# Kernel tuning notes

Hardware: AMD Instinct MI355X
Metric: run time of the kernel (lower is better)

## Reference

```python
import jax, jax.numpy as jnp
import numpy as np

# Forest of B complete binary trees, depth DEPTH (root at level 0, leaves at level DEPTH)
B = 16
DEPTH = 14
NPT = 2 ** (DEPTH + 1) - 1   # nodes per tree = 32767
N = B * NPT                  # total nodes = 524272
X = 128                      # x_size
H = 128                      # h_size
NC = 10                      # num_classes


def _tree_levels():
    """Static tree structure: per internal level, (node_ids, children_ids[.,2]); plus leaf ids."""
    offs = np.arange(B, dtype=np.int64)[:, None] * NPT
    levels = []
    for l in range(DEPTH):  # internal levels 0..DEPTH-1
        n = np.arange(2 ** l - 1, 2 ** (l + 1) - 1, dtype=np.int64)
        ch = np.stack([2 * n + 1, 2 * n + 2], axis=1)
        nodes = (n[None, :] + offs).reshape(-1)
        children = (ch[None, :, :] + offs[:, :, None]).reshape(-1, 2)
        levels.append((nodes, children))
    leaf = np.arange(2 ** DEPTH - 1, NPT, dtype=np.int64)
    leaves = (leaf[None, :] + offs).reshape(-1)
    return levels, leaves


def _apply_node(iou, c_in):
    # iou: [M, 3H]; chunk order i, o, u as in torch.chunk(iou, 3, 1)
    i, o, u = jnp.split(iou, 3, axis=-1)
    c = jax.nn.sigmoid(i) * jnp.tanh(u) + c_in
    h = jax.nn.sigmoid(o) * jnp.tanh(c)
    return h, c


def setup_inputs() -> dict:
    key = jax.random.key(0)
    ks = jax.random.split(key, 8)
    rn = lambda k, shp, sc: jax.random.normal(k, shp, dtype=jnp.float32) * sc
    return {
        "feature": rn(ks[0], (N, X), 1.0),
        "h": rn(ks[1], (N, H), 1.0),
        "c": rn(ks[2], (N, H), 1.0),
        "W_iou": rn(ks[3], (3 * H, X), 0.05),
        "U_iou": rn(ks[4], (3 * H, H), 0.05),
        "b_iou": jnp.zeros((1, 3 * H), jnp.float32),
        "U_f_w": rn(ks[5], (H, H), 0.05),
        "U_f_b": jnp.zeros((H,), jnp.float32),
        "W_lin": rn(ks[6], (NC, H), 0.05),
        "b_lin": jnp.zeros((NC,), jnp.float32),
    }


def reference(feature, h, c, W_iou, U_iou, b_iou, U_f_w, U_f_b, W_lin, b_lin):
    levels, leaves = _tree_levels()

    # Leaves: no mailbox -> iou = W_iou(x) + b_iou, c stays initial c
    iou_leaf = feature[leaves] @ W_iou.T + b_iou
    h_leaf, c_leaf = _apply_node(iou_leaf, c[leaves])
    h = h.at[leaves].set(h_leaf)
    c = c.at[leaves].set(c_leaf)

    # Internal levels bottom-up (topological order)
    for nodes, children in reversed(levels):
        hc = h[children]                                  # [M, 2, H]
        cc = c[children]                                  # [M, 2, H]
        h_tild = hc.sum(axis=1)                           # child-sum
        f = jax.nn.sigmoid(jnp.einsum('mkh,gh->mkg', hc, U_f_w) + U_f_b)
        c_agg = (f * cc).sum(axis=1)
        # DGL reduce OVERWRITES 'iou': internal nodes use U_iou(h_tild) only
        iou = h_tild @ U_iou.T + b_iou
        h_new, c_new = _apply_node(iou, c_agg)
        h = h.at[nodes].set(h_new)
        c = c.at[nodes].set(c_new)

    # AvgPooling over each graph's nodes, then classifier
    hg = h.reshape(B, NPT, H).mean(axis=1)
    logits = hg @ W_lin.T + b_lin
    return jax.nn.log_softmax(logits, axis=-1)
```

## Files before the change

### kernel.cpp

```cpp
#include <hip/hip_runtime.h>
#include <hip/hip_bf16.h>
#include <stdint.h>

#define NTREES 16
#define TDEPTH 14
#define NPT    32767
#define HDIM   128

typedef __bf16 bf16x8 __attribute__((ext_vector_type(8)));
typedef float  f32x4  __attribute__((ext_vector_type(4)));

__device__ __forceinline__ float fsig(float x) {
    return __builtin_amdgcn_rcpf(1.0f + __expf(-x));
}
__device__ __forceinline__ float ftanh(float x) {
    return 1.0f - 2.0f * __builtin_amdgcn_rcpf(__expf(2.0f * x) + 1.0f);
}

__global__ __launch_bounds__(256) void prep_kernel(
    const float* __restrict__ W_iou, const float* __restrict__ U_iou,
    const float* __restrict__ U_f,
    __bf16* __restrict__ wiou_bf, __bf16* __restrict__ uiou_bf,
    __bf16* __restrict__ uf_bf, float* __restrict__ hg)
{
    int idx = blockIdx.x * 256 + threadIdx.x;
    if (idx < 49152)       wiou_bf[idx]          = (__bf16)W_iou[idx];
    else if (idx < 98304)  uiou_bf[idx - 49152]  = (__bf16)U_iou[idx - 49152];
    else if (idx < 114688) uf_bf[idx - 98304]    = (__bf16)U_f[idx - 98304];
    else if (idx < 116736) hg[idx - 114688]      = 0.0f;
}

__global__ __launch_bounds__(256) void leaf_kernel(
    const float* __restrict__ feat, float* __restrict__ c,
    const __bf16* __restrict__ wiou_bf, const float* __restrict__ b_iou,
    __bf16* __restrict__ hbf)
{
    __shared__ __align__(16) __bf16 As[128 * 128];
    const int t = threadIdx.x;
    const int blk = blockIdx.x;
    const int tree = blk >> 7, chunk = blk & 127;
    const int rowbase = tree * NPT + 16383 + chunk * 128;

    for (int idx = t; idx < 128 * 32; idx += 256) {
        int r = idx >> 5, c4 = idx & 31;
        const float4 v = *reinterpret_cast<const float4*>(
            feat + (size_t)(rowbase + r) * HDIM + c4 * 4);
        int u16 = (c4 >> 1) ^ (r & 7);
        __bf16* dst = As + r * 128 + u16 * 8 + (c4 & 1) * 4;
        dst[0] = (__bf16)v.x; dst[1] = (__bf16)v.y;
        dst[2] = (__bf16)v.z; dst[3] = (__bf16)v.w;
    }
    __syncthreads();

    const int wave = t >> 6, lane = t & 63;
    const int n15 = lane & 15, q = lane >> 4;
    int aoff[4];
    #pragma unroll
    for (int kk = 0; kk < 4; ++kk) aoff[kk] = ((kk * 4 + q) ^ (n15 & 7)) * 8;

    for (int jj = 0; jj < 2; ++jj) {
        const int jg = wave + jj * 4;
        bf16x8 bfr[3][4];
        #pragma unroll
        for (int p = 0; p < 3; ++p) {
            const __bf16* bp = wiou_bf + (size_t)(p * 128 + jg * 16 + n15) * HDIM + q * 8;
            #pragma unroll
            for (int kk = 0; kk < 4; ++kk)
                bfr[p][kk] = *reinterpret_cast<const bf16x8*>(bp + kk * 32);
        }
        const int j = jg * 16 + n15;
        const float bi = b_iou[j], bo = b_iou[128 + j], bu = b_iou[256 + j];
        for (int mt = 0; mt < 8; ++mt) {
            bf16x8 afr[4];
            #pragma unroll
            for (int kk = 0; kk < 4; ++kk)
                afr[kk] = *reinterpret_cast<const bf16x8*>(As + (mt * 16 + n15) * 128 + aoff[kk]);
            f32x4 ai = {0,0,0,0}, ao = {0,0,0,0}, au = {0,0,0,0};
            #pragma unroll
            for (int kk = 0; kk < 4; ++kk) {
                ai = __builtin_amdgcn_mfma_f32_16x16x32_bf16(afr[kk], bfr[0][kk], ai, 0,0,0);
                ao = __builtin_amdgcn_mfma_f32_16x16x32_bf16(afr[kk], bfr[1][kk], ao, 0,0,0);
                au = __builtin_amdgcn_mfma_f32_16x16x32_bf16(afr[kk], bfr[2][kk], au, 0,0,0);
            }
            #pragma unroll
            for (int reg = 0; reg < 4; ++reg) {
                int r = mt * 16 + q * 4 + reg;
                size_t off = (size_t)(rowbase + r) * HDIM + j;
                float ci = c[off];
                float cn = fsig(ai[reg] + bi) * ftanh(au[reg] + bu) + ci;
                float hn = fsig(ao[reg] + bo) * ftanh(cn);
                c[off]   = cn;
                hbf[off] = (__bf16)hn;
            }
        }
    }
}

__global__ __launch_bounds__(256) void level_kernel(
    int l, int Mlev,
    float* __restrict__ c,
    const __bf16* __restrict__ uiou_bf, const __bf16* __restrict__ uf_bf,
    const float* __restrict__ b_iou, const float* __restrict__ ufb,
    __bf16* __restrict__ hbf)
{
    __shared__ __align__(16) __bf16 Hc[64 * 128];
    __shared__ __align__(16) __bf16 Ht[32 * 128];
    __shared__ float cagg[32 * 132];
    const int t = threadIdx.x;
    const int blk32 = blockIdx.x * 32;
    const int nmask = (1 << l) - 1;

    for (int idx = t; idx < 64 * 16; idx += 256) {
        int r = idx >> 4, s = idx & 15;
        int inode = blk32 + (r >> 1);
        uint4 v = {0, 0, 0, 0};
        if (inode < Mlev) {
            int tree = inode >> l, local = inode & nmask;
            int nloc = nmask + local;
            size_t crow = (size_t)tree * NPT + 2 * nloc + 1 + (r & 1);
            v = *reinterpret_cast<const uint4*>(hbf + crow * HDIM + s * 8);
        }
        *reinterpret_cast<uint4*>(Hc + r * 128 + ((s ^ (r & 7)) * 8)) = v;
    }
    __syncthreads();

    for (int idx = t; idx < 32 * 16; idx += 256) {
        int nno = idx >> 4, s = idx & 15;
        const __bf16* p0 = Hc + (2 * nno)     * 128 + ((s ^ ((2 * nno) & 7)) * 8);
        const __bf16* p1 = Hc + (2 * nno + 1) * 128 + ((s ^ ((2 * nno + 1) & 7)) * 8);
        __bf16* po = Ht + nno * 128 + ((s ^ (nno & 7)) * 8);
        #pragma unroll
        for (int e = 0; e < 8; ++e) po[e] = (__bf16)((float)p0[e] + (float)p1[e]);
    }
    __syncthreads();

    const int wave = t >> 6, lane = t & 63;
    const int n15 = lane & 15, q = lane >> 4;
    int aoff[4];
    #pragma unroll
    for (int kk = 0; kk < 4; ++kk) aoff[kk] = ((kk * 4 + q) ^ (n15 & 7)) * 8;

    {
        bf16x8 bfr[2][4];
        #pragma unroll
        for (int i = 0; i < 2; ++i) {
            int nt = wave + i * 4;
            const __bf16* bp = uf_bf + (size_t)(nt * 16 + n15) * HDIM + q * 8;
            #pragma unroll
            for (int kk = 0; kk < 4; ++kk)
                bfr[i][kk] = *reinterpret_cast<const bf16x8*>(bp + kk * 32);
        }
        for (int mt = 0; mt < 4; ++mt) {
            bf16x8 afr[4];
            #pragma unroll
            for (int kk = 0; kk < 4; ++kk)
                afr[kk] = *reinterpret_cast<const bf16x8*>(Hc + (mt * 16 + n15) * 128 + aoff[kk]);
            f32x4 acc0 = {0,0,0,0}, acc1 = {0,0,0,0};
            #pragma unroll
            for (int kk = 0; kk < 4; ++kk) {
                acc0 = __builtin_amdgcn_mfma_f32_16x16x32_bf16(afr[kk], bfr[0][kk], acc0, 0,0,0);
                acc1 = __builtin_amdgcn_mfma_f32_16x16x32_bf16(afr[kk], bfr[1][kk], acc1, 0,0,0);
            }
            #pragma unroll
            for (int i = 0; i < 2; ++i) {
                int nt = wave + i * 4;
                int j = nt * 16 + n15;
                float fb = ufb[j];
                f32x4 acc = i ? acc1 : acc0;
                #pragma unroll
                for (int p = 0; p < 2; ++p) {
                    int nl = mt * 8 + q * 2 + p;
                    int inode = blk32 + nl;
                    if (inode < Mlev) {
                        int tree = inode >> l, local = inode & nmask;
                        int nloc = nmask + local;
                        size_t crow = (size_t)tree * NPT + 2 * nloc + 1;
                        float c0 = c[crow * HDIM + j];
                        float c1 = c[(crow + 1) * HDIM + j];
                        float f0 = fsig(acc[2 * p] + fb);
                        float f1 = fsig(acc[2 * p + 1] + fb);
                        cagg[nl * 132 + j] = f0 * c0 + f1 * c1;
                    }
                }
            }
        }
    }
    __syncthreads();

    for (int jj = 0; jj < 2; ++jj) {
        const int jg = wave + jj * 4;
        bf16x8 bfr[3][4];
        #pragma unroll
        for (int p = 0; p < 3; ++p) {
            const __bf16* bp = uiou_bf + (size_t)(p * 128 + jg * 16 + n15) * HDIM + q * 8;
            #pragma unroll
            for (int kk = 0; kk < 4; ++kk)
                bfr[p][kk] = *reinterpret_cast<const bf16x8*>(bp + kk * 32);
        }
        const int j = jg * 16 + n15;
        const float bi = b_iou[j], bo = b_iou[128 + j], bu = b_iou[256 + j];
        for (int mt = 0; mt < 2; ++mt) {
            bf16x8 afr[4];
            #pragma unroll
            for (int kk = 0; kk < 4; ++kk)
                afr[kk] = *reinterpret_cast<const bf16x8*>(Ht + (mt * 16 + n15) * 128 + aoff[kk]);
            f32x4 ai = {0,0,0,0}, ao = {0,0,0,0}, au = {0,0,0,0};
            #pragma unroll
            for (int kk = 0; kk < 4; ++kk) {
                ai = __builtin_amdgcn_mfma_f32_16x16x32_bf16(afr[kk], bfr[0][kk], ai, 0,0,0);
                ao = __builtin_amdgcn_mfma_f32_16x16x32_bf16(afr[kk], bfr[1][kk], ao, 0,0,0);
                au = __builtin_amdgcn_mfma_f32_16x16x32_bf16(afr[kk], bfr[2][kk], au, 0,0,0);
            }
            #pragma unroll
            for (int reg = 0; reg < 4; ++reg) {
                int nl = mt * 16 + q * 4 + reg;
                int inode = blk32 + nl;
                if (inode < Mlev) {
                    int tree = inode >> l, local = inode & nmask;
                    int nloc = nmask + local;
                    size_t nrow = (size_t)tree * NPT + nloc;
                    float cg = cagg[nl * 132 + j];
                    float cn = fsig(ai[reg] + bi) * ftanh(au[reg] + bu) + cg;
                    float hn = fsig(ao[reg] + bo) * ftanh(cn);
                    c[nrow * HDIM + j]   = cn;
                    hbf[nrow * HDIM + j] = (__bf16)hn;
                }
            }
        }
    }
}

__global__ __launch_bounds__(256) void pool_kernel(
    const __bf16* __restrict__ hbf, float* __restrict__ hg)
{
    const int t = threadIdx.x;
    const int tree = blockIdx.x >> 6, chunk = blockIdx.x & 63;
    const int col = t & 127, rg = t >> 7;
    const int r0 = chunk * 512;
    const int r1 = (r0 + 512 < NPT) ? (r0 + 512) : NPT;
    float s = 0.0f;
    for (int row = r0 + rg; row < r1; row += 2)
        s += (float)hbf[((size_t)tree * NPT + row) * HDIM + col];
    atomicAdd(&hg[tree * HDIM + col], s);
}

__global__ __launch_bounds__(256) void cls_kernel(
    const float* __restrict__ hg, const float* __restrict__ W_lin,
    const float* __restrict__ b_lin, float* __restrict__ out)
{
    __shared__ float lg[16 * 10];
    const int t = threadIdx.x;
    if (t < 160) {
        int b = t / 10, cc = t % 10;
        float s = b_lin[cc];
        const float inv = 1.0f / 32767.0f;
        for (int j = 0; j < HDIM; ++j)
            s += hg[b * HDIM + j] * inv * W_lin[cc * HDIM + j];
        lg[b * 10 + cc] = s;
    }
    __syncthreads();
    if (t < 16) {
        float m = lg[t * 10];
        for (int i = 1; i < 10; ++i) m = fmaxf(m, lg[t * 10 + i]);
        float sum = 0.0f;
        for (int i = 0; i < 10; ++i) sum += __expf(lg[t * 10 + i] - m);
        float lse = __logf(sum) + m;
        for (int i = 0; i < 10; ++i) out[t * 10 + i] = lg[t * 10 + i] - lse;
    }
}

extern "C" void kernel_launch(void* const* d_in, const int* in_sizes, int n_in,
                              void* d_out, int out_size, void* d_ws, size_t ws_size,
                              hipStream_t stream)
{
    const float* feat  = (const float*)d_in[0];
    char*        hbase = (char*)d_in[1];
    float*       c     = (float*)d_in[2];
    const float* W_iou = (const float*)d_in[3];
    const float* U_iou = (const float*)d_in[4];
    const float* b_iou = (const float*)d_in[5];
    const float* U_f_w = (const float*)d_in[6];
    const float* U_f_b = (const float*)d_in[7];
    const float* W_lin = (const float*)d_in[8];
    const float* b_lin = (const float*)d_in[9];

    __bf16* hbf = (__bf16*)hbase;
    const size_t WOFF = 134217728;
    __bf16* wiou_bf = (__bf16*)(hbase + WOFF);
    __bf16* uiou_bf = (__bf16*)(hbase + WOFF + 98304);
    __bf16* uf_bf   = (__bf16*)(hbase + WOFF + 196608);
    float*  hg      = (float*)(hbase + WOFF + 229376);

    prep_kernel<<<456, 256, 0, stream>>>(W_iou, U_iou, U_f_w, wiou_bf, uiou_bf, uf_bf, hg);
    leaf_kernel<<<2048, 256, 0, stream>>>(feat, c, wiou_bf, b_iou, hbf);
    for (int l = TDEPTH - 1; l >= 0; --l) {
        int Mlev = NTREES << l;
        int grid = (Mlev + 31) / 32;
        level_kernel<<<grid, 256, 0, stream>>>(l, Mlev, c, uiou_bf, uf_bf, b_iou, U_f_b, hbf);
    }
    pool_kernel<<<1024, 256, 0, stream>>>(hbf, hg);
    cls_kernel<<<1, 256, 0, stream>>>(hg, W_lin, b_lin, (float*)d_out);
}
```

Baseline: 1.165 ms.

## Fuse leaves and two lowest internal levels in shared memory, fuse pooling and tail levels

```diff
diff --git a/kernel.cpp b/kernel.cpp
--- a/kernel.cpp
+++ b/kernel.cpp
@@ -3,9 +3,7 @@
 #include <stdint.h>
 
 #define NTREES 16
-#define TDEPTH 14
 #define NPT    32767
-#define HDIM   128
 
 typedef __bf16 bf16x8 __attribute__((ext_vector_type(8)));
 typedef float  f32x4  __attribute__((ext_vector_type(4)));
@@ -15,6 +13,9 @@
 }
 __device__ __forceinline__ float ftanh(float x) {
     return 1.0f - 2.0f * __builtin_amdgcn_rcpf(__expf(2.0f * x) + 1.0f);
+}
+__device__ __forceinline__ int swz(int r, int j) {
+    return r * 128 + (((j >> 3) ^ (r & 7)) << 3) + (j & 7);
 }
 
 __global__ __launch_bounds__(256) void prep_kernel(
@@ -30,47 +31,62 @@
     else if (idx < 116736) hg[idx - 114688]      = 0.0f;
 }
 
-__global__ __launch_bounds__(256) void leaf_kernel(
-    const float* __restrict__ feat, float* __restrict__ c,
-    const __bf16* __restrict__ wiou_bf, const float* __restrict__ b_iou,
-    __bf16* __restrict__ hbf)
+__global__ __launch_bounds__(256) void mega_kernel(
+    const float* __restrict__ feat, const float* __restrict__ c0g,
+    const __bf16* __restrict__ wiou, const __bf16* __restrict__ uiou,
+    const __bf16* __restrict__ uf,
+    const float* __restrict__ b_iou, const float* __restrict__ ufb,
+    __bf16* __restrict__ hbf, __bf16* __restrict__ cbf, float* __restrict__ hg)
 {
-    __shared__ __align__(16) __bf16 As[128 * 128];
+    __shared__ __align__(16) __bf16 HA[64 * 128];
+    __shared__ __align__(16) __bf16 CA[64 * 136];
+    __shared__ __align__(16) unsigned char Sbuf[8192 + 32 * 132 * 4];
+    __bf16* As   = (__bf16*)Sbuf;
+    __bf16* Ht   = (__bf16*)Sbuf;
+    float*  cagg = (float*)(Sbuf + 8192);
+
     const int t = threadIdx.x;
-    const int blk = blockIdx.x;
-    const int tree = blk >> 7, chunk = blk & 127;
-    const int rowbase = tree * NPT + 16383 + chunk * 128;
-
-    for (int idx = t; idx < 128 * 32; idx += 256) {
+    const int tree = blockIdx.x >> 8, sub = blockIdx.x & 255;
+    const size_t leafrow = (size_t)tree * NPT + 16383 + (size_t)sub * 64;
+
+    for (int idx = t; idx < 64 * 32; idx += 256) {
         int r = idx >> 5, c4 = idx & 31;
-        const float4 v = *reinterpret_cast<const float4*>(
-            feat + (size_t)(rowbase + r) * HDIM + c4 * 4);
-        int u16 = (c4 >> 1) ^ (r & 7);
-        __bf16* dst = As + r * 128 + u16 * 8 + (c4 & 1) * 4;
-        dst[0] = (__bf16)v.x; dst[1] = (__bf16)v.y;
-        dst[2] = (__bf16)v.z; dst[3] = (__bf16)v.w;
-    }
-    __syncthreads();
-
-    const int wave = t >> 6, lane = t & 63;
-    const int n15 = lane & 15, q = lane >> 4;
+        float4 v = *reinterpret_cast<const float4*>(feat + (leafrow + r) * 128 + c4 * 4);
+        __bf16* dst = As + r * 128 + (((c4 >> 1) ^ (r & 7)) << 3) + ((c4 & 1) << 2);
+        dst[0] = (__bf16)v.x; dst[1] = (__bf16)v.y; dst[2] = (__bf16)v.z; dst[3] = (__bf16)v.w;
+    }
+    __syncthreads();
+
+    const int wave = t >> 6, lane = t & 63, n15 = lane & 15, q = lane >> 4;
     int aoff[4];
     #pragma unroll
-    for (int kk = 0; kk < 4; ++kk) aoff[kk] = ((kk * 4 + q) ^ (n15 & 7)) * 8;
-
+    for (int kk = 0; kk < 4; ++kk) aoff[kk] = ((kk * 4 + q) ^ (n15 & 7)) << 3;
+    float hsum0 = 0.f, hsum1 = 0.f;
+
+    bf16x8 ufr[2][4];
+    float fb[2];
+    #pragma unroll
+    for (int i = 0; i < 2; ++i) {
+        int nt = wave + i * 4;
+        const __bf16* bp = uf + (size_t)(nt * 16 + n15) * 128 + q * 8;
+        #pragma unroll
+        for (int kk = 0; kk < 4; ++kk) ufr[i][kk] = *reinterpret_cast<const bf16x8*>(bp + kk * 32);
+        fb[i] = ufb[nt * 16 + n15];
+    }
+
+    #pragma unroll
     for (int jj = 0; jj < 2; ++jj) {
         const int jg = wave + jj * 4;
         bf16x8 bfr[3][4];
         #pragma unroll
         for (int p = 0; p < 3; ++p) {
-            const __bf16* bp = wiou_bf + (size_t)(p * 128 + jg * 16 + n15) * HDIM + q * 8;
-            #pragma unroll
-            for (int kk = 0; kk < 4; ++kk)
-                bfr[p][kk] = *reinterpret_cast<const bf16x8*>(bp + kk * 32);
+            const __bf16* bp = wiou + (size_t)(p * 128 + jg * 16 + n15) * 128 + q * 8;
+            #pragma unroll
+            for (int kk = 0; kk < 4; ++kk) bfr[p][kk] = *reinterpret_cast<const bf16x8*>(bp + kk * 32);
         }
         const int j = jg * 16 + n15;
         const float bi = b_iou[j], bo = b_iou[128 + j], bu = b_iou[256 + j];
-        for (int mt = 0; mt < 8; ++mt) {
+        for (int mt = 0; mt < 4; ++mt) {
             bf16x8 afr[4];
             #pragma unroll
             for (int kk = 0; kk < 4; ++kk)
@@ -85,23 +101,169 @@
             #pragma unroll
             for (int reg = 0; reg < 4; ++reg) {
                 int r = mt * 16 + q * 4 + reg;
-                size_t off = (size_t)(rowbase + r) * HDIM + j;
-                float ci = c[off];
+                float ci = c0g[(leafrow + r) * 128 + j];
                 float cn = fsig(ai[reg] + bi) * ftanh(au[reg] + bu) + ci;
                 float hn = fsig(ao[reg] + bo) * ftanh(cn);
-                c[off]   = cn;
-                hbf[off] = (__bf16)hn;
-            }
-        }
-    }
+                HA[swz(r, j)]    = (__bf16)hn;
+                CA[r * 136 + j]  = (__bf16)cn;
+                if (jj == 0) hsum0 += hn; else hsum1 += hn;
+            }
+        }
+    }
+    __syncthreads();
+
+    for (int idx = t; idx < 32 * 16; idx += 256) {
+        int nno = idx >> 4, s = idx & 15;
+        const __bf16* p0 = HA + (2 * nno) * 128     + (((s ^ ((2 * nno) & 7))) << 3);
+        const __bf16* p1 = HA + (2 * nno + 1) * 128 + (((s ^ ((2 * nno + 1) & 7))) << 3);
+        __bf16* po = Ht + nno * 128 + (((s ^ (nno & 7))) << 3);
+        #pragma unroll
+        for (int e = 0; e < 8; ++e) po[e] = (__bf16)((float)p0[e] + (float)p1[e]);
+    }
+    for (int mt = 0; mt < 4; ++mt) {
+        bf16x8 afr[4];
+        #pragma unroll
+        for (int kk = 0; kk < 4; ++kk)
+            afr[kk] = *reinterpret_cast<const bf16x8*>(HA + (mt * 16 + n15) * 128 + aoff[kk]);
+        f32x4 a0 = {0,0,0,0}, a1 = {0,0,0,0};
+        #pragma unroll
+        for (int kk = 0; kk < 4; ++kk) {
+            a0 = __builtin_amdgcn_mfma_f32_16x16x32_bf16(afr[kk], ufr[0][kk], a0, 0,0,0);
+            a1 = __builtin_amdgcn_mfma_f32_16x16x32_bf16(afr[kk], ufr[1][kk], a1, 0,0,0);
+        }
+        #pragma unroll
+        for (int i = 0; i < 2; ++i) {
+            int j2 = (wave + i * 4) * 16 + n15;
+            f32x4 acc = i ? a1 : a0;
+            #pragma unroll
+            for (int p = 0; p < 2; ++p) {
+                int nl = mt * 8 + q * 2 + p;
+                float cc0 = (float)CA[(2 * nl) * 136 + j2];
+                float cc1 = (float)CA[(2 * nl + 1) * 136 + j2];
+                cagg[nl * 132 + j2] = fsig(acc[2*p] + fb[i]) * cc0 + fsig(acc[2*p+1] + fb[i]) * cc1;
+            }
+        }
+    }
+    __syncthreads();
+    #pragma unroll
+    for (int jj = 0; jj < 2; ++jj) {
+        const int jg = wave + jj * 4;
+        bf16x8 bfr[3][4];
+        #pragma unroll
+        for (int p = 0; p < 3; ++p) {
+            const __bf16* bp = uiou + (size_t)(p * 128 + jg * 16 + n15) * 128 + q * 8;
+            #pragma unroll
+            for (int kk = 0; kk < 4; ++kk) bfr[p][kk] = *reinterpret_cast<const bf16x8*>(bp + kk * 32);
+        }
+        const int j = jg * 16 + n15;
+        const float bi = b_iou[j], bo = b_iou[128 + j], bu = b_iou[256 + j];
+        for (int mt = 0; mt < 2; ++mt) {
+            bf16x8 afr[4];
+            #pragma unroll
+            for (int kk = 0; kk < 4; ++kk)
+                afr[kk] = *reinterpret_cast<const bf16x8*>(Ht + (mt * 16 + n15) * 128 + aoff[kk]);
+            f32x4 ai = {0,0,0,0}, ao = {0,0,0,0}, au = {0,0,0,0};
+            #pragma unroll
+            for (int kk = 0; kk < 4; ++kk) {
+                ai = __builtin_amdgcn_mfma_f32_16x16x32_bf16(afr[kk], bfr[0][kk], ai, 0,0,0);
+                ao = __builtin_amdgcn_mfma_f32_16x16x32_bf16(afr[kk], bfr[1][kk], ao, 0,0,0);
+                au = __builtin_amdgcn_mfma_f32_16x16x32_bf16(afr[kk], bfr[2][kk], au, 0,0,0);
+            }
+            #pragma unroll
+            for (int reg = 0; reg < 4; ++reg) {
+                int nl = mt * 16 + q * 4 + reg;
+                float cg = cagg[nl * 132 + j];
+                float cn = fsig(ai[reg] + bi) * ftanh(au[reg] + bu) + cg;
+                float hn = fsig(ao[reg] + bo) * ftanh(cn);
+                HA[swz(nl, j)]    = (__bf16)hn;
+                CA[nl * 136 + j]  = (__bf16)cn;
+                if (jj == 0) hsum0 += hn; else hsum1 += hn;
+            }
+        }
+    }
+    __syncthreads();
+
+    for (int idx = t; idx < 16 * 16; idx += 256) {
+        int nno = idx >> 4, s = idx & 15;
+        const __bf16* p0 = HA + (2 * nno) * 128     + (((s ^ ((2 * nno) & 7))) << 3);
+        const __bf16* p1 = HA + (2 * nno + 1) * 128 + (((s ^ ((2 * nno + 1) & 7))) << 3);
+        __bf16* po = Ht + nno * 128 + (((s ^ (nno & 7))) << 3);
+        #pragma unroll
+        for (int e = 0; e < 8; ++e) po[e] = (__bf16)((float)p0[e] + (float)p1[e]);
+    }
+    for (int mt = 0; mt < 2; ++mt) {
+        bf16x8 afr[4];
+        #pragma unroll
+        for (int kk = 0; kk < 4; ++kk)
+            afr[kk] = *reinterpret_cast<const bf16x8*>(HA + (mt * 16 + n15) * 128 + aoff[kk]);
+        f32x4 a0 = {0,0,0,0}, a1 = {0,0,0,0};
+        #pragma unroll
+        for (int kk = 0; kk < 4; ++kk) {
+            a0 = __builtin_amdgcn_mfma_f32_16x16x32_bf16(afr[kk], ufr[0][kk], a0, 0,0,0);
+            a1 = __builtin_amdgcn_mfma_f32_16x16x32_bf16(afr[kk], ufr[1][kk], a1, 0,0,0);
+        }
+        #pragma unroll
+        for (int i = 0; i < 2; ++i) {
+            int j2 = (wave + i * 4) * 16 + n15;
+            f32x4 acc = i ? a1 : a0;
+            #pragma unroll
+            for (int p = 0; p < 2; ++p) {
+                int nl = mt * 8 + q * 2 + p;
+                float cc0 = (float)CA[(2 * nl) * 136 + j2];
+                float cc1 = (float)CA[(2 * nl + 1) * 136 + j2];
+                cagg[nl * 132 + j2] = fsig(acc[2*p] + fb[i]) * cc0 + fsig(acc[2*p+1] + fb[i]) * cc1;
+            }
+        }
+    }
+    __syncthreads();
+    const size_t p12row = (size_t)tree * NPT + 4095 + (size_t)sub * 16;
+    #pragma unroll
+    for (int jj = 0; jj < 2; ++jj) {
+        const int jg = wave + jj * 4;
+        bf16x8 bfr[3][4];
+        #pragma unroll
+        for (int p = 0; p < 3; ++p) {
+            const __bf16* bp = uiou + (size_t)(p * 128 + jg * 16 + n15) * 128 + q * 8;
+            #pragma unroll
+            for (int kk = 0; kk < 4; ++kk) bfr[p][kk] = *reinterpret_cast<const bf16x8*>(bp + kk * 32);
+        }
+        const int j = jg * 16 + n15;
+        const float bi = b_iou[j], bo = b_iou[128 + j], bu = b_iou[256 + j];
+        bf16x8 afr[4];
+        #pragma unroll
+        for (int kk = 0; kk < 4; ++kk)
+            afr[kk] = *reinterpret_cast<const bf16x8*>(Ht + n15 * 128 + aoff[kk]);
+        f32x4 ai = {0,0,0,0}, ao = {0,0,0,0}, au = {0,0,0,0};
+        #pragma unroll
+        for (int kk = 0; kk < 4; ++kk) {
+            ai = __builtin_amdgcn_mfma_f32_16x16x32_bf16(afr[kk], bfr[0][kk], ai, 0,0,0);
+            ao = __builtin_amdgcn_mfma_f32_16x16x32_bf16(afr[kk], bfr[1][kk], ao, 0,0,0);
+            au = __builtin_amdgcn_mfma_f32_16x16x32_bf16(afr[kk], bfr[2][kk], au, 0,0,0);
+        }
+        #pragma unroll
+        for (int reg = 0; reg < 4; ++reg) {
+            int nl = q * 4 + reg;
+            float cg = cagg[nl * 132 + j];
+            float cn = fsig(ai[reg] + bi) * ftanh(au[reg] + bu) + cg;
+            float hn = fsig(ao[reg] + bo) * ftanh(cn);
+            cbf[(p12row + nl) * 128 + j] = (__bf16)cn;
+            hbf[(p12row + nl) * 128 + j] = (__bf16)hn;
+            if (jj == 0) hsum0 += hn; else hsum1 += hn;
+        }
+    }
+
+    float v = hsum0;
+    v += __shfl_xor(v, 16); v += __shfl_xor(v, 32);
+    if (lane < 16) atomicAdd(&hg[tree * 128 + wave * 16 + lane], v);
+    v = hsum1;
+    v += __shfl_xor(v, 16); v += __shfl_xor(v, 32);
+    if (lane < 16) atomicAdd(&hg[tree * 128 + (wave + 4) * 16 + lane], v);
 }
 
 __global__ __launch_bounds__(256) void level_kernel(
-    int l, int Mlev,
-    float* __restrict__ c,
-    const __bf16* __restrict__ uiou_bf, const __bf16* __restrict__ uf_bf,
+    int l, const __bf16* __restrict__ uiou, const __bf16* __restrict__ uf,
     const float* __restrict__ b_iou, const float* __restrict__ ufb,
-    __bf16* __restrict__ hbf)
+    __bf16* __restrict__ hbf, __bf16* __restrict__ cbf, float* __restrict__ hg)
 {
     __shared__ __align__(16) __bf16 Hc[64 * 128];
     __shared__ __align__(16) __bf16 Ht[32 * 128];
@@ -113,89 +275,74 @@
     for (int idx = t; idx < 64 * 16; idx += 256) {
         int r = idx >> 4, s = idx & 15;
         int inode = blk32 + (r >> 1);
-        uint4 v = {0, 0, 0, 0};
-        if (inode < Mlev) {
-            int tree = inode >> l, local = inode & nmask;
-            int nloc = nmask + local;
-            size_t crow = (size_t)tree * NPT + 2 * nloc + 1 + (r & 1);
-            v = *reinterpret_cast<const uint4*>(hbf + crow * HDIM + s * 8);
-        }
-        *reinterpret_cast<uint4*>(Hc + r * 128 + ((s ^ (r & 7)) * 8)) = v;
-    }
-    __syncthreads();
-
+        int tree = inode >> l, local = inode & nmask;
+        size_t crow = (size_t)tree * NPT + 2 * (nmask + local) + 1 + (r & 1);
+        uint4 v = *reinterpret_cast<const uint4*>(hbf + crow * 128 + s * 8);
+        *reinterpret_cast<uint4*>(Hc + r * 128 + ((s ^ (r & 7)) << 3)) = v;
+    }
+    __syncthreads();
     for (int idx = t; idx < 32 * 16; idx += 256) {
         int nno = idx >> 4, s = idx & 15;
-        const __bf16* p0 = Hc + (2 * nno)     * 128 + ((s ^ ((2 * nno) & 7)) * 8);
-        const __bf16* p1 = Hc + (2 * nno + 1) * 128 + ((s ^ ((2 * nno + 1) & 7)) * 8);
-        __bf16* po = Ht + nno * 128 + ((s ^ (nno & 7)) * 8);
+        const __bf16* p0 = Hc + (2 * nno) * 128     + (((s ^ ((2 * nno) & 7))) << 3);
+        const __bf16* p1 = Hc + (2 * nno + 1) * 128 + (((s ^ ((2 * nno + 1) & 7))) << 3);
+        __bf16* po = Ht + nno * 128 + (((s ^ (nno & 7))) << 3);
         #pragma unroll
         for (int e = 0; e < 8; ++e) po[e] = (__bf16)((float)p0[e] + (float)p1[e]);
     }
-    __syncthreads();
-
-    const int wave = t >> 6, lane = t & 63;
-    const int n15 = lane & 15, q = lane >> 4;
+
+    const int wave = t >> 6, lane = t & 63, n15 = lane & 15, q = lane >> 4;
     int aoff[4];
     #pragma unroll
-    for (int kk = 0; kk < 4; ++kk) aoff[kk] = ((kk * 4 + q) ^ (n15 & 7)) * 8;
-
-    {
-        bf16x8 bfr[2][4];
+    for (int kk = 0; kk < 4; ++kk) aoff[kk] = ((kk * 4 + q) ^ (n15 & 7)) << 3;
+    float hsum0 = 0.f, hsum1 = 0.f;
+
+    bf16x8 ufr[2][4];
+    float fb[2];
+    #pragma unroll
+    for (int i = 0; i < 2; ++i) {
+        int nt = wave + i * 4;
+        const __bf16* bp = uf + (size_t)(nt * 16 + n15) * 128 + q * 8;
+        #pragma unroll
+        for (int kk = 0; kk < 4; ++kk) ufr[i][kk] = *reinterpret_cast<const bf16x8*>(bp + kk * 32);
+        fb[i] = ufb[nt * 16 + n15];
+    }
+    for (int mt = 0; mt < 4; ++mt) {
+        bf16x8 afr[4];
+        #pragma unroll
+        for (int kk = 0; kk < 4; ++kk)
+            afr[kk] = *reinterpret_cast<const bf16x8*>(Hc + (mt * 16 + n15) * 128 + aoff[kk]);
+        f32x4 a0 = {0,0,0,0}, a1 = {0,0,0,0};
+        #pragma unroll
+        for (int kk = 0; kk < 4; ++kk) {
+            a0 = __builtin_amdgcn_mfma_f32_16x16x32_bf16(afr[kk], ufr[0][kk], a0, 0,0,0);
+            a1 = __builtin_amdgcn_mfma_f32_16x16x32_bf16(afr[kk], ufr[1][kk], a1, 0,0,0);
+        }
         #pragma unroll
         for (int i = 0; i < 2; ++i) {
-            int nt = wave + i * 4;
-            const __bf16* bp = uf_bf + (size_t)(nt * 16 + n15) * HDIM + q * 8;
-            #pragma unroll
-            for (int kk = 0; kk < 4; ++kk)
-                bfr[i][kk] = *reinterpret_cast<const bf16x8*>(bp + kk * 32);
-        }
-        for (int mt = 0; mt < 4; ++mt) {
-            bf16x8 afr[4];
-            #pragma unroll
-            for (int kk = 0; kk < 4; ++kk)
-                afr[kk] = *reinterpret_cast<const bf16x8*>(Hc + (mt * 16 + n15) * 128 + aoff[kk]);
-            f32x4 acc0 = {0,0,0,0}, acc1 = {0,0,0,0};
-            #pragma unroll
-            for (int kk = 0; kk < 4; ++kk) {
-                acc0 = __builtin_amdgcn_mfma_f32_16x16x32_bf16(afr[kk], bfr[0][kk], acc0, 0,0,0);
-                acc1 = __builtin_amdgcn_mfma_f32_16x16x32_bf16(afr[kk], bfr[1][kk], acc1, 0,0,0);
-            }
-            #pragma unroll
-            for (int i = 0; i < 2; ++i) {
-                int nt = wave + i * 4;
-                int j = nt * 16 + n15;
-                float fb = ufb[j];
-                f32x4 acc = i ? acc1 : acc0;
-                #pragma unroll
-                for (int p = 0; p < 2; ++p) {
-                    int nl = mt * 8 + q * 2 + p;
-                    int inode = blk32 + nl;
-                    if (inode < Mlev) {
-                        int tree = inode >> l, local = inode & nmask;
-                        int nloc = nmask + local;
-                        size_t crow = (size_t)tree * NPT + 2 * nloc + 1;
-                        float c0 = c[crow * HDIM + j];
-                        float c1 = c[(crow + 1) * HDIM + j];
-                        float f0 = fsig(acc[2 * p] + fb);
-                        float f1 = fsig(acc[2 * p + 1] + fb);
-                        cagg[nl * 132 + j] = f0 * c0 + f1 * c1;
-                    }
-                }
-            }
-        }
-    }
-    __syncthreads();
-
+            int j2 = (wave + i * 4) * 16 + n15;
+            f32x4 acc = i ? a1 : a0;
+            #pragma unroll
+            for (int p = 0; p < 2; ++p) {
+                int nl = mt * 8 + q * 2 + p;
+                int inode = blk32 + nl;
+                int tree = inode >> l, local = inode & nmask;
+                size_t crow = (size_t)tree * NPT + 2 * (nmask + local) + 1;
+                float cc0 = (float)cbf[crow * 128 + j2];
+                float cc1 = (float)cbf[(crow + 1) * 128 + j2];
+                cagg[nl * 132 + j2] = fsig(acc[2*p] + fb[i]) * cc0 + fsig(acc[2*p+1] + fb[i]) * cc1;
+            }
+        }
+    }
+    __syncthreads();
+    #pragma unroll
     for (int jj = 0; jj < 2; ++jj) {
         const int jg = wave + jj * 4;
         bf16x8 bfr[3][4];
         #pragma unroll
         for (int p = 0; p < 3; ++p) {
-            const __bf16* bp = uiou_bf + (size_t)(p * 128 + jg * 16 + n15) * HDIM + q * 8;
-            #pragma unroll
-            for (int kk = 0; kk < 4; ++kk)
-                bfr[p][kk] = *reinterpret_cast<const bf16x8*>(bp + kk * 32);
+            const __bf16* bp = uiou + (size_t)(p * 128 + jg * 16 + n15) * 128 + q * 8;
+            #pragma unroll
+            for (int kk = 0; kk < 4; ++kk) bfr[p][kk] = *reinterpret_cast<const bf16x8*>(bp + kk * 32);
         }
         const int j = jg * 16 + n15;
         const float bi = b_iou[j], bo = b_iou[128 + j], bu = b_iou[256 + j];
@@ -215,33 +362,153 @@
             for (int reg = 0; reg < 4; ++reg) {
                 int nl = mt * 16 + q * 4 + reg;
                 int inode = blk32 + nl;
-                if (inode < Mlev) {
-                    int tree = inode >> l, local = inode & nmask;
-                    int nloc = nmask + local;
-                    size_t nrow = (size_t)tree * NPT + nloc;
-                    float cg = cagg[nl * 132 + j];
+                int tree = inode >> l, local = inode & nmask;
+                size_t nrow = (size_t)tree * NPT + nmask + local;
+                float cg = cagg[nl * 132 + j];
+                float cn = fsig(ai[reg] + bi) * ftanh(au[reg] + bu) + cg;
+                float hn = fsig(ao[reg] + bo) * ftanh(cn);
+                cbf[nrow * 128 + j] = (__bf16)cn;
+                hbf[nrow * 128 + j] = (__bf16)hn;
+                if (jj == 0) hsum0 += hn; else hsum1 += hn;
+            }
+        }
+    }
+    const int tree0 = blk32 >> l;
+    float v = hsum0;
+    v += __shfl_xor(v, 16); v += __shfl_xor(v, 32);
+    if (lane < 16) atomicAdd(&hg[tree0 * 128 + wave * 16 + lane], v);
+    v = hsum1;
+    v += __shfl_xor(v, 16); v += __shfl_xor(v, 32);
+    if (lane < 16) atomicAdd(&hg[tree0 * 128 + (wave + 4) * 16 + lane], v);
+}
+
+__global__ __launch_bounds__(256) void tail_kernel(
+    const __bf16* __restrict__ uiou, const __bf16* __restrict__ uf,
+    const float* __restrict__ b_iou, const float* __restrict__ ufb,
+    const __bf16* __restrict__ hbf, const __bf16* __restrict__ cbf,
+    float* __restrict__ hg)
+{
+    __shared__ __align__(16) __bf16 Hp[2][32 * 128];
+    __shared__ __align__(16) __bf16 Cp[2][32 * 136];
+    __shared__ __align__(16) __bf16 HtT[16 * 128];
+    __shared__ float caggT[16 * 132];
+    const int t = threadIdx.x;
+    const int tree = blockIdx.x;
+    const size_t base5 = (size_t)tree * NPT + 31;
+
+    for (int idx = t; idx < 32 * 16; idx += 256) {
+        int r = idx >> 4, s = idx & 15;
+        uint4 v = *reinterpret_cast<const uint4*>(hbf + (base5 + r) * 128 + s * 8);
+        *reinterpret_cast<uint4*>(Hp[0] + r * 128 + ((s ^ (r & 7)) << 3)) = v;
+        uint4 w = *reinterpret_cast<const uint4*>(cbf + (base5 + r) * 128 + s * 8);
+        *reinterpret_cast<uint4*>(Cp[0] + r * 136 + s * 8) = w;
+    }
+    __syncthreads();
+
+    const int wave = t >> 6, lane = t & 63, n15 = lane & 15, q = lane >> 4;
+    int aoff[4];
+    #pragma unroll
+    for (int kk = 0; kk < 4; ++kk) aoff[kk] = ((kk * 4 + q) ^ (n15 & 7)) << 3;
+    float hsum0 = 0.f, hsum1 = 0.f;
+
+    bf16x8 ufr[2][4];
+    float fb[2];
+    #pragma unroll
+    for (int i = 0; i < 2; ++i) {
+        int nt = wave + i * 4;
+        const __bf16* bp = uf + (size_t)(nt * 16 + n15) * 128 + q * 8;
+        #pragma unroll
+        for (int kk = 0; kk < 4; ++kk) ufr[i][kk] = *reinterpret_cast<const bf16x8*>(bp + kk * 32);
+        fb[i] = ufb[nt * 16 + n15];
+    }
+
+    int cur = 0;
+    for (int l = 4; l >= 0; --l) {
+        const int M = 1 << l;
+        __bf16* Hin  = Hp[cur];     __bf16* Cin  = Cp[cur];
+        __bf16* Hout = Hp[cur ^ 1]; __bf16* Cout = Cp[cur ^ 1];
+        for (int idx = t; idx < M * 16; idx += 256) {
+            int nno = idx >> 4, s = idx & 15;
+            const __bf16* p0 = Hin + (2 * nno) * 128     + (((s ^ ((2 * nno) & 7))) << 3);
+            const __bf16* p1 = Hin + (2 * nno + 1) * 128 + (((s ^ ((2 * nno + 1) & 7))) << 3);
+            __bf16* po = HtT + nno * 128 + (((s ^ (nno & 7))) << 3);
+            #pragma unroll
+            for (int e = 0; e < 8; ++e) po[e] = (__bf16)((float)p0[e] + (float)p1[e]);
+        }
+        const int mtF = (2 * M + 15) >> 4;
+        for (int mt = 0; mt < mtF; ++mt) {
+            bf16x8 afr[4];
+            #pragma unroll
+            for (int kk = 0; kk < 4; ++kk)
+                afr[kk] = *reinterpret_cast<const bf16x8*>(Hin + (mt * 16 + n15) * 128 + aoff[kk]);
+            f32x4 a0 = {0,0,0,0}, a1 = {0,0,0,0};
+            #pragma unroll
+            for (int kk = 0; kk < 4; ++kk) {
+                a0 = __builtin_amdgcn_mfma_f32_16x16x32_bf16(afr[kk], ufr[0][kk], a0, 0,0,0);
+                a1 = __builtin_amdgcn_mfma_f32_16x16x32_bf16(afr[kk], ufr[1][kk], a1, 0,0,0);
+            }
+            #pragma unroll
+            for (int i = 0; i < 2; ++i) {
+                int j2 = (wave + i * 4) * 16 + n15;
+                f32x4 acc = i ? a1 : a0;
+                #pragma unroll
+                for (int p = 0; p < 2; ++p) {
+                    int nl = mt * 8 + q * 2 + p;
+                    if (nl < M) {
+                        float cc0 = (float)Cin[(2 * nl) * 136 + j2];
+                        float cc1 = (float)Cin[(2 * nl + 1) * 136 + j2];
+                        caggT[nl * 132 + j2] = fsig(acc[2*p] + fb[i]) * cc0
+                                             + fsig(acc[2*p+1] + fb[i]) * cc1;
+                    }
+                }
+            }
+        }
+        __syncthreads();
+        #pragma unroll
+        for (int jj = 0; jj < 2; ++jj) {
+            const int jg = wave + jj * 4;
+            bf16x8 bfr[3][4];
+            #pragma unroll
+            for (int p = 0; p < 3; ++p) {
+                const __bf16* bp = uiou + (size_t)(p * 128 + jg * 16 + n15) * 128 + q * 8;
+                #pragma unroll
+                for (int kk = 0; kk < 4; ++kk) bfr[p][kk] = *reinterpret_cast<const bf16x8*>(bp + kk * 32);
+            }
+            const int j = jg * 16 + n15;
+            const float bi = b_iou[j], bo = b_iou[128 + j], bu = b_iou[256 + j];
+            bf16x8 afr[4];
+            #pragma unroll
+            for (int kk = 0; kk < 4; ++kk)
+                afr[kk] = *reinterpret_cast<const bf16x8*>(HtT + n15 * 128 + aoff[kk]);
+            f32x4 ai = {0,0,0,0}, ao = {0,0,0,0}, au = {0,0,0,0};
+            #pragma unroll
+            for (int kk = 0; kk < 4; ++kk) {
+                ai = __builtin_amdgcn_mfma_f32_16x16x32_bf16(afr[kk], bfr[0][kk], ai, 0,0,0);
+                ao = __builtin_amdgcn_mfma_f32_16x16x32_bf16(afr[kk], bfr[1][kk], ao, 0,0,0);
+                au = __builtin_amdgcn_mfma_f32_16x16x32_bf16(afr[kk], bfr[2][kk], au, 0,0,0);
+            }
+            #pragma unroll
+            for (int reg = 0; reg < 4; ++reg) {
+                int nl = q * 4 + reg;
+                if (nl < M) {
+                    float cg = caggT[nl * 132 + j];
                     float cn = fsig(ai[reg] + bi) * ftanh(au[reg] + bu) + cg;
                     float hn = fsig(ao[reg] + bo) * ftanh(cn);
-                    c[nrow * HDIM + j]   = cn;
-                    hbf[nrow * HDIM + j] = (__bf16)hn;
+                    Hout[swz(nl, j)]   = (__bf16)hn;
+                    Cout[nl * 136 + j] = (__bf16)cn;
+                    if (jj == 0) hsum0 += hn; else hsum1 += hn;
                 }
             }
         }
-    }
-}
-
-__global__ __launch_bounds__(256) void pool_kernel(
-    const __bf16* __restrict__ hbf, float* __restrict__ hg)
-{
-    const int t = threadIdx.x;
-    const int tree = blockIdx.x >> 6, chunk = blockIdx.x & 63;
-    const int col = t & 127, rg = t >> 7;
-    const int r0 = chunk * 512;
-    const int r1 = (r0 + 512 < NPT) ? (r0 + 512) : NPT;
-    float s = 0.0f;
-    for (int row = r0 + rg; row < r1; row += 2)
-        s += (float)hbf[((size_t)tree * NPT + row) * HDIM + col];
-    atomicAdd(&hg[tree * HDIM + col], s);
+        __syncthreads();
+        cur ^= 1;
+    }
+    float v = hsum0;
+    v += __shfl_xor(v, 16); v += __shfl_xor(v, 32);
+    if (lane < 16) atomicAdd(&hg[tree * 128 + wave * 16 + lane], v);
+    v = hsum1;
+    v += __shfl_xor(v, 16); v += __shfl_xor(v, 32);
+    if (lane < 16) atomicAdd(&hg[tree * 128 + (wave + 4) * 16 + lane], v);
 }
 
 __global__ __launch_bounds__(256) void cls_kernel(
@@ -254,8 +521,8 @@
         int b = t / 10, cc = t % 10;
         float s = b_lin[cc];
         const float inv = 1.0f / 32767.0f;
-        for (int j = 0; j < HDIM; ++j)
-            s += hg[b * HDIM + j] * inv * W_lin[cc * HDIM + j];
+        for (int j = 0; j < 128; ++j)
+            s += hg[b * 128 + j] * inv * W_lin[cc * 128 + j];
         lg[b * 10 + cc] = s;
     }
     __syncthreads();
@@ -274,8 +541,7 @@
                               hipStream_t stream)
 {
     const float* feat  = (const float*)d_in[0];
-    char*        hbase = (char*)d_in[1];
-    float*       c     = (float*)d_in[2];
+    const float* c0g   = (const float*)d_in[2];
     const float* W_iou = (const float*)d_in[3];
     const float* U_iou = (const float*)d_in[4];
     const float* b_iou = (const float*)d_in[5];
@@ -284,20 +550,20 @@
     const float* W_lin = (const float*)d_in[8];
     const float* b_lin = (const float*)d_in[9];
 
-    __bf16* hbf = (__bf16*)hbase;
-    const size_t WOFF = 134217728;
-    __bf16* wiou_bf = (__bf16*)(hbase + WOFF);
-    __bf16* uiou_bf = (__bf16*)(hbase + WOFF + 98304);
-    __bf16* uf_bf   = (__bf16*)(hbase + WOFF + 196608);
-    float*  hg      = (float*)(hbase + WOFF + 229376);
+    char* ws = (char*)d_ws;
+    __bf16* hbf     = (__bf16*)ws;
+    __bf16* cbf     = (__bf16*)(ws + 134217728);
+    __bf16* wiou_bf = (__bf16*)(ws + 268435456);
+    __bf16* uiou_bf = (__bf16*)(ws + 268435456 + 98304);
+    __bf16* uf_bf   = (__bf16*)(ws + 268435456 + 196608);
+    float*  hg      = (float*)(ws + 268435456 + 229376);
 
     prep_kernel<<<456, 256, 0, stream>>>(W_iou, U_iou, U_f_w, wiou_bf, uiou_bf, uf_bf, hg);
-    leaf_kernel<<<2048, 256, 0, stream>>>(feat, c, wiou_bf, b_iou, hbf);
-    for (int l = TDEPTH - 1; l >= 0; --l) {
-        int Mlev = NTREES << l;
-        int grid = (Mlev + 31) / 32;
-        level_kernel<<<grid, 256, 0, stream>>>(l, Mlev, c, uiou_bf, uf_bf, b_iou, U_f_b, hbf);
-    }
-    pool_kernel<<<1024, 256, 0, stream>>>(hbf, hg);
+    mega_kernel<<<4096, 256, 0, stream>>>(feat, c0g, wiou_bf, uiou_bf, uf_bf,
+                                          b_iou, U_f_b, hbf, cbf, hg);
+    for (int l = 11; l >= 5; --l)
+        level_kernel<<<(NTREES << l) / 32, 256, 0, stream>>>(l, uiou_bf, uf_bf,
+                                                             b_iou, U_f_b, hbf, cbf, hg);
+    tail_kernel<<<16, 256, 0, stream>>>(uiou_bf, uf_bf, b_iou, U_f_b, hbf, cbf, hg);
     cls_kernel<<<1, 256, 0, stream>>>(hg, W_lin, b_lin, (float*)d_out);
 }
```

Result: faster. 938.8 us (-19.4%).
